# Kernel tuning notes

Measured on AMD Instinct MI355X. Metric: run time of the kernel, lower is better.

The kernel has to match this reference:

```python
import jax, jax.numpy as jnp
import numpy as np

H = 16        # num heads
DH = 128      # head dim
C = 64        # delta-rule chunk size
MAG = 0.5     # mag_weight
GATE_NORM = 16.0
EPS = 1e-6


def setup_inputs() -> dict:
    key = jax.random.key(0)
    ks = jax.random.split(key, 5)
    b, n, d = 2, 1024, H * DH
    s = d ** -0.5
    return {
        "x": jax.random.normal(ks[0], (b, n, d), jnp.float32),
        "Wq": jax.random.normal(ks[1], (d, d), jnp.float32) * s,
        "Wk": jax.random.normal(ks[2], (d, d), jnp.float32) * s,
        "Wv": jax.random.normal(ks[3], (d, d), jnp.float32) * s,
        "Wo": jax.random.normal(ks[4], (d, d), jnp.float32) * s,
    }


def _delta_rule_chunkwise(q, k, v, beta, chunk):
    # q,k,v: [b,h,l,d]; beta: [b,h,l,d] per-dim gate. Chunked DeltaNet parallel form.
    b, h, l, dk = q.shape
    dv = v.shape[-1]
    nc = l // chunk
    q = q * (dk ** -0.5)
    v = v * beta
    k_beta = k * beta
    qc, kc, vc, kbc = (a.reshape(b, h, nc, chunk, -1) for a in (q, k, v, k_beta))
    eye = jnp.eye(chunk, dtype=q.dtype)
    strict = jnp.tril(jnp.ones((chunk, chunk), bool), -1)
    # T = (I + strict_lower(k_beta k^T))^{-1} via triangular solve
    L = jnp.where(strict, kbc @ jnp.swapaxes(kc, -1, -2), 0.0)  # [b,h,nc,C,C]
    T = jax.scipy.linalg.solve_triangular(eye + L, jnp.broadcast_to(eye, L.shape), lower=True)
    u = T @ vc    # [b,h,nc,C,dv]
    w = T @ kbc   # [b,h,nc,C,dk]
    incl = jnp.tril(jnp.ones((chunk, chunk), bool))

    def step(S, inp):
        q_i, k_i, u_i, w_i = inp  # [b,h,C,d]
        u_i = u_i - w_i @ S
        attn = jnp.where(incl, q_i @ jnp.swapaxes(k_i, -1, -2), 0.0)
        o_i = q_i @ S + attn @ u_i
        S = S + jnp.swapaxes(k_i, -1, -2) @ u_i
        return S, o_i

    xs = tuple(jnp.moveaxis(a, 2, 0) for a in (qc, kc, u, w))
    S0 = jnp.zeros((b, h, dk, dv), q.dtype)
    S, o = jax.lax.scan(step, S0, xs)
    o = jnp.moveaxis(o, 0, 2).reshape(b, h, l, dv)
    return o, S


def _heads(t, b, n):
    return t.reshape(b, n, H, DH).transpose(0, 2, 1, 3)


def _base_attn(x, Wq, Wk, Wv, Wo):
    # vanilla causal softmax attention using the shared projections
    b, n, d = x.shape
    q, k, v = _heads(x @ Wq, b, n), _heads(x @ Wk, b, n), _heads(x @ Wv, b, n)
    scores = jnp.einsum('bhqd,bhkd->bhqk', q, k) / np.sqrt(DH).astype(np.float32)
    causal = jnp.tril(jnp.ones((n, n), bool))
    a = jax.nn.softmax(jnp.where(causal, scores, -jnp.inf), axis=-1)
    o = jnp.einsum('bhqk,bhkd->bhqd', a, v)
    return o.transpose(0, 2, 1, 3).reshape(b, n, d) @ Wo


def reference(x, Wq, Wk, Wv, Wo):
    b, n, d = x.shape
    k_raw = x @ Wk
    q = _heads(x @ Wq, b, n)
    k = _heads(k_raw, b, n)
    v = _heads(x @ Wv, b, n)
    g = _heads(k_raw, b, n)  # pool_g is identity: output_size == head_dim*num_kv_heads
    q = jnp.clip(jax.nn.softmax(q, axis=-1), EPS, 1.0 - EPS)
    k = jnp.clip(jax.nn.softmax(k, axis=-1), EPS, 1.0 - EPS)
    g = jnp.clip(jax.nn.log_sigmoid(g) / GATE_NORM, -GATE_NORM, GATE_NORM)
    o_lin, _ = _delta_rule_chunkwise(q.astype(jnp.float32), k.astype(jnp.float32),
                                     v.astype(jnp.float32), g.astype(jnp.float32), C)
    o_lin = o_lin.transpose(0, 2, 1, 3).reshape(b, n, d) @ Wo
    o_base = _base_attn(x, Wq, Wk, Wv, Wo)
    return MAG * o_lin + (1.0 - MAG) * o_base
```

## Files before the change

### kernel.cpp

```cpp
#include <hip/hip_runtime.h>
#include <hip/hip_bf16.h>
#include <math.h>

#define D 2048
#define NROWS 2048
#define NQKV 6144
#define H 16
#define DH 128
#define CHK 64
#define NC 16
#define EPSC 1e-6f
#define RSQDH 0.08838834764831845f

typedef unsigned short ushort_t;
typedef __attribute__((ext_vector_type(4))) float f4_t;
typedef __attribute__((ext_vector_type(8))) short s8_t;
typedef __attribute__((ext_vector_type(8))) _Float16 h8_t;
typedef __attribute__((ext_vector_type(4))) _Float16 h4_t;
typedef __attribute__((ext_vector_type(2))) _Float16 h2_t;
typedef __attribute__((ext_vector_type(4))) unsigned short us4_t;
typedef __attribute__((ext_vector_type(2))) unsigned short us2_t;

#define MFMA16(a, b, c) __builtin_amdgcn_mfma_f32_16x16x32_bf16((a), (b), (c), 0, 0, 0)
#define MFMAH(a, b, c)  __builtin_amdgcn_mfma_f32_16x16x32_f16((a), (b), (c), 0, 0, 0)
#define GLOAD16(g, l) __builtin_amdgcn_global_load_lds((const __attribute__((address_space(1))) unsigned int*)(g), (__attribute__((address_space(3))) unsigned int*)(l), 16, 0, 0)

__device__ __forceinline__ ushort_t f2bf(float f) {
  union { float f; unsigned u; } v; v.f = f;
  unsigned r = (v.u + 0x7fffu + ((v.u >> 16) & 1u)) >> 16;
  return (ushort_t)r;
}
__device__ __forceinline__ float bf2f(ushort_t h) {
  union { unsigned u; float f; } v; v.u = ((unsigned)h) << 16;
  return v.f;
}

__global__ __launch_bounds__(256) void split_h(const float* __restrict__ in,
                                               _Float16* __restrict__ hi) {
  int i = (blockIdx.x * 256 + threadIdx.x) * 4;
  float4 v = *(const float4*)(in + i);
  float vv[4] = {v.x, v.y, v.z, v.w};
  h4_t h;
#pragma unroll
  for (int j = 0; j < 4; j++) h[j] = (_Float16)vv[j];
  *(h4_t*)(hi + i) = h;
}

__global__ __launch_bounds__(256) void wsplit4(const float* __restrict__ Wq,
                                               const float* __restrict__ Wk,
                                               const float* __restrict__ Wv,
                                               const float* __restrict__ Wo,
                                               _Float16* __restrict__ Tqkv,
                                               _Float16* __restrict__ To) {
  __shared__ float t[32][33];
  const int tid = threadIdx.x;
  const int k0 = blockIdx.y * 32, n0 = blockIdx.x * 32;
  const int z = blockIdx.z;
  const float* W = (z == 0) ? Wq : (z == 1) ? Wk : (z == 2) ? Wv : Wo;
  _Float16* T = (z < 3) ? (Tqkv + (size_t)z * D * D) : To;
  const int c = tid & 31, rr = tid >> 5;
#pragma unroll
  for (int p = 0; p < 4; p++) {
    int r = p * 8 + rr;
    t[r][c] = W[(size_t)(k0 + r) * D + n0 + c];
  }
  __syncthreads();
#pragma unroll
  for (int p = 0; p < 4; p++) {
    int r = p * 8 + rr;
    T[(size_t)(n0 + r) * D + k0 + c] = (_Float16)t[c][r];
  }
}

__global__ __launch_bounds__(256) void gemm1(const _Float16* __restrict__ Ah,
                                             const _Float16* __restrict__ Bt,
                                             float* __restrict__ C,
                                             int M, int N, int K) {
  __shared__ __align__(16) ushort_t A_s[2][4096];
  __shared__ __align__(16) ushort_t B_s[2][4096];
  const int tid = threadIdx.x, lane = tid & 63, wid = tid >> 6;
  const int nwg = gridDim.x;
  int bid = blockIdx.x;
  int swz = (bid & 7) * (nwg >> 3) + (bid >> 3);
  const int nbn = N >> 7;
  const int bm = swz / nbn, bn = swz % nbn;
  const int row0 = bm << 7, col0 = bn << 7;
  const int lm = lane & 15, lg = lane >> 4;
  const int wrow = (wid >> 1) * 64, wcol = (wid & 1) * 64;
  const int NT = K >> 5;

  f4_t acc[4][4];
#pragma unroll
  for (int m = 0; m < 4; m++)
#pragma unroll
    for (int n = 0; n < 4; n++) acc[m][n] = (f4_t){0.f, 0.f, 0.f, 0.f};

  auto stage = [&](int buf, int ks) {
    int k0 = ks << 5;
#pragma unroll
    for (int p = 0; p < 2; p++) {
      int c = p * 256 + wid * 64 + lane;
      int r = c >> 2, q = (c & 3) * 8;
      char* la = (char*)&A_s[buf][0] + p * 4096 + wid * 1024;
      GLOAD16(Ah + (size_t)(row0 + r) * K + k0 + q, la);
      char* lb = (char*)&B_s[buf][0] + p * 4096 + wid * 1024;
      GLOAD16(Bt + (size_t)(col0 + r) * K + k0 + q, lb);
    }
  };

  stage(0, 0);
  __syncthreads();
  for (int t = 0; t < NT; t++) {
    int cur = t & 1;
    if (t + 1 < NT) stage(cur ^ 1, t + 1);
    h8_t af[4], bfr[4];
#pragma unroll
    for (int m = 0; m < 4; m++)
      af[m] = *(const h8_t*)&A_s[cur][(wrow + m * 16 + lm) * 32 + lg * 8];
#pragma unroll
    for (int n = 0; n < 4; n++)
      bfr[n] = *(const h8_t*)&B_s[cur][(wcol + n * 16 + lm) * 32 + lg * 8];
#pragma unroll
    for (int m = 0; m < 4; m++)
#pragma unroll
      for (int n = 0; n < 4; n++)
        acc[m][n] = MFMAH(af[m], bfr[n], acc[m][n]);
    __syncthreads();
  }
#pragma unroll
  for (int m = 0; m < 4; m++)
#pragma unroll
    for (int n = 0; n < 4; n++)
#pragma unroll
      for (int r = 0; r < 4; r++)
        C[(size_t)(row0 + wrow + m * 16 + lg * 4 + r) * N + col0 + wcol + n * 16 + lm] = acc[m][n][r];
}

__global__ __launch_bounds__(256) void gemm1h(const _Float16* __restrict__ Ah,
                                              const _Float16* __restrict__ Bt,
                                              _Float16* __restrict__ C,
                                              int M, int N, int K) {
  __shared__ __align__(16) ushort_t A_s[2][4096];
  __shared__ __align__(16) ushort_t B_s[2][4096];
  const int tid = threadIdx.x, lane = tid & 63, wid = tid >> 6;
  const int nwg = gridDim.x;
  int bid = blockIdx.x;
  int swz = (bid & 7) * (nwg >> 3) + (bid >> 3);
  const int nbn = N >> 7;
  const int bm = swz / nbn, bn = swz % nbn;
  const int lm = lane & 15, lg = lane >> 4;
  const int row0 = bm << 7, col0 = bn << 7;
  const int wrow = (wid >> 1) * 64, wcol = (wid & 1) * 64;
  const int NT = K >> 5;

  f4_t acc[4][4];
#pragma unroll
  for (int m = 0; m < 4; m++)
#pragma unroll
    for (int n = 0; n < 4; n++) acc[m][n] = (f4_t){0.f, 0.f, 0.f, 0.f};

  auto stage = [&](int buf, int ks) {
    int k0 = ks << 5;
#pragma unroll
    for (int p = 0; p < 2; p++) {
      int c = p * 256 + wid * 64 + lane;
      int r = c >> 2, q = (c & 3) * 8;
      char* la = (char*)&A_s[buf][0] + p * 4096 + wid * 1024;
      GLOAD16(Ah + (size_t)(row0 + r) * K + k0 + q, la);
      char* lb = (char*)&B_s[buf][0] + p * 4096 + wid * 1024;
      GLOAD16(Bt + (size_t)(col0 + r) * K + k0 + q, lb);
    }
  };

  stage(0, 0);
  __syncthreads();
  for (int t = 0; t < NT; t++) {
    int cur = t & 1;
    if (t + 1 < NT) stage(cur ^ 1, t + 1);
    h8_t af[4], bfr[4];
#pragma unroll
    for (int m = 0; m < 4; m++)
      af[m] = *(const h8_t*)&A_s[cur][(wrow + m * 16 + lm) * 32 + lg * 8];
#pragma unroll
    for (int n = 0; n < 4; n++)
      bfr[n] = *(const h8_t*)&B_s[cur][(wcol + n * 16 + lm) * 32 + lg * 8];
#pragma unroll
    for (int m = 0; m < 4; m++)
#pragma unroll
      for (int n = 0; n < 4; n++)
        acc[m][n] = MFMAH(af[m], bfr[n], acc[m][n]);
    __syncthreads();
  }
#pragma unroll
  for (int m = 0; m < 4; m++)
#pragma unroll
    for (int n = 0; n < 4; n++)
#pragma unroll
      for (int r = 0; r < 4; r++)
        C[(size_t)(row0 + wrow + m * 16 + lg * 4 + r) * N + col0 + wcol + n * 16 + lm] = (_Float16)acc[m][n][r];
}

__device__ __forceinline__ float gate_fn(float z) {
  float t = -z;
  float sp = (t > 20.f) ? t : log1pf(expf(t));
  float g = -sp * (1.f / 16.f);
  return fminf(fmaxf(g, -16.f), 16.f);
}

__global__ __launch_bounds__(256) void act_kernel(const _Float16* __restrict__ qkv,
                                                  ushort_t* __restrict__ qs_h,
                                                  ushort_t* __restrict__ qs_l,
                                                  float* __restrict__ ksm,
                                                  float* __restrict__ kb,
                                                  float* __restrict__ vb,
                                                  ushort_t* __restrict__ qb16,
                                                  ushort_t* __restrict__ kb16) {
  int wave = blockIdx.x * 4 + (threadIdx.x >> 6);
  int lane = threadIdx.x & 63;
  int row = wave >> 4, h = wave & 15;
  size_t inb = (size_t)row * NQKV + h * 128;
  size_t base = (size_t)wave * 128;
  const int e0 = 2 * lane;

  h2_t qv = *(const h2_t*)(qkv + inb + e0);
  h2_t kv = *(const h2_t*)(qkv + inb + 2048 + e0);
  h2_t vv = *(const h2_t*)(qkv + inb + 4096 + e0);
  float q0 = (float)qv[0], q1 = (float)qv[1];
  float k0 = (float)kv[0], k1 = (float)kv[1];
  float v0 = (float)vv[0], v1 = (float)vv[1];

  us2_t qo = {f2bf(q0 * RSQDH), f2bf(q1 * RSQDH)};
  us2_t ko = {f2bf(k0), f2bf(k1)};
  *(us2_t*)(qb16 + base + e0) = qo;
  *(us2_t*)(kb16 + base + e0) = ko;

  float m = fmaxf(q0, q1);
  for (int o = 1; o < 64; o <<= 1) m = fmaxf(m, __shfl_xor(m, o));
  float e0f = expf(q0 - m), e1f = expf(q1 - m);
  float s = e0f + e1f;
  for (int o = 1; o < 64; o <<= 1) s += __shfl_xor(s, o);
  float inv = 1.f / s;
  float qs0 = fminf(fmaxf(e0f * inv, EPSC), 1.f - EPSC) * RSQDH;
  float qs1 = fminf(fmaxf(e1f * inv, EPSC), 1.f - EPSC) * RSQDH;

  float mk = fmaxf(k0, k1);
  for (int o = 1; o < 64; o <<= 1) mk = fmaxf(mk, __shfl_xor(mk, o));
  float f0 = expf(k0 - mk), f1 = expf(k1 - mk);
  float sk = f0 + f1;
  for (int o = 1; o < 64; o <<= 1) sk += __shfl_xor(sk, o);
  float invk = 1.f / sk;
  float ks0 = fminf(fmaxf(f0 * invk, EPSC), 1.f - EPSC);
  float ks1 = fminf(fmaxf(f1 * invk, EPSC), 1.f - EPSC);

  float g0 = gate_fn(k0), g1 = gate_fn(k1);

  ushort_t qh0 = f2bf(qs0), qh1 = f2bf(qs1);
  us2_t qhv = {qh0, qh1};
  us2_t qlv = {f2bf(qs0 - bf2f(qh0)), f2bf(qs1 - bf2f(qh1))};
  *(us2_t*)(qs_h + base + e0) = qhv;
  *(us2_t*)(qs_l + base + e0) = qlv;

  *(float2*)(ksm + base + e0) = make_float2(ks0, ks1);
  *(float2*)(kb + base + e0) = make_float2(ks0 * g0, ks1 * g1);
  *(float2*)(vb + base + e0) = make_float2(v0 * g0, v1 * g1);
}

__global__ __launch_bounds__(256) void chunk_uw_kernel(const ushort_t* __restrict__ qs_h,
                                                       const ushort_t* __restrict__ qs_l,
                                                       const float* __restrict__ ksm,
                                                       const float* __restrict__ kb,
                                                       const float* __restrict__ vb,
                                                       float* __restrict__ u,
                                                       ushort_t* __restrict__ w_h,
                                                       ushort_t* __restrict__ w_l,
                                                       ushort_t* __restrict__ attn_h,
                                                       ushort_t* __restrict__ attn_l,
                                                       ushort_t* __restrict__ kTh_g,
                                                       ushort_t* __restrict__ kTl_g) {
  __shared__ __align__(16) ushort_t kh_s[8192];
  __shared__ __align__(16) ushort_t kl_s[8192];
  __shared__ __align__(16) ushort_t xh_s[8192];
  __shared__ __align__(16) ushort_t xl_s[8192];
  __shared__ float L_s[4096];
  const int tid = threadIdx.x, lane = tid & 63, wid = tid >> 6;
  const int lm = lane & 15, lg = lane >> 4;
  const int bh = blockIdx.x >> 4, ci = blockIdx.x & 15;
  const int rowbase = (bh >> 4) * 1024 + ci * 64;
  const int colbase = (bh & 15) * 128;
  const size_t gbase = (size_t)rowbase * D + colbase;
  const int wr = (wid >> 1) * 32, wc = (wid & 1) * 32;

  auto stageM = [&](const float* __restrict__ src, ushort_t* dh, ushort_t* dl) {
#pragma unroll
    for (int it = 0; it < 4; it++) {
      int idx = tid + it * 256;
      int r = idx >> 4, c8 = idx & 15;
      const float* g = src + gbase + (size_t)r * D + c8 * 8;
      float4 v0 = *(const float4*)g;
      float4 v1 = *(const float4*)(g + 4);
      float vv[8] = {v0.x, v0.y, v0.z, v0.w, v1.x, v1.y, v1.z, v1.w};
      s8_t hv, lv;
#pragma unroll
      for (int j = 0; j < 8; j++) {
        ushort_t hb = f2bf(vv[j]);
        hv[j] = (short)hb;
        lv[j] = (short)f2bf(vv[j] - bf2f(hb));
      }
      int byo = r * 256 + ((c8 * 16) ^ ((r & 7) << 4));
      *(s8_t*)((char*)dh + byo) = hv;
      *(s8_t*)((char*)dl + byo) = lv;
    }
  };

  auto stageHL = [&](const ushort_t* __restrict__ srcH,
                     const ushort_t* __restrict__ srcL,
                     ushort_t* dh, ushort_t* dl) {
#pragma unroll
    for (int it = 0; it < 4; it++) {
      int idx = tid + it * 256;
      int r = idx >> 4, c8 = idx & 15;
      size_t g = gbase + (size_t)r * D + c8 * 8;
      s8_t hv = *(const s8_t*)(srcH + g);
      s8_t lv = *(const s8_t*)(srcL + g);
      int byo = r * 256 + ((c8 * 16) ^ ((r & 7) << 4));
      *(s8_t*)((char*)dh + byo) = hv;
      *(s8_t*)((char*)dl + byo) = lv;
    }
  };

  auto mm3 = [&](const ushort_t* Ah, const ushort_t* Al,
                 const ushort_t* Bh, const ushort_t* Bl, f4_t acc[2][2]) {
#pragma unroll
    for (int m = 0; m < 2; m++)
#pragma unroll
      for (int n = 0; n < 2; n++) acc[m][n] = (f4_t){0.f, 0.f, 0.f, 0.f};
#pragma unroll
    for (int term = 0; term < 3; term++) {
      const ushort_t* A = (term == 2) ? Al : Ah;
      const ushort_t* Bsrc = (term == 1) ? Bl : Bh;
#pragma unroll
      for (int ks = 0; ks < 4; ks++) {
        s8_t af[2], bf_[2];
#pragma unroll
        for (int m = 0; m < 2; m++) {
          int row = wr + m * 16 + lm;
          int byo = row * 256 + ((ks * 64 + lg * 16) ^ ((row & 7) << 4));
          af[m] = *(const s8_t*)((const char*)A + byo);
        }
#pragma unroll
        for (int n = 0; n < 2; n++) {
          int row = wc + n * 16 + lm;
          int byo = row * 256 + ((ks * 64 + lg * 16) ^ ((row & 7) << 4));
          bf_[n] = *(const s8_t*)((const char*)Bsrc + byo);
        }
#pragma unroll
        for (int m = 0; m < 2; m++)
#pragma unroll
          for (int n = 0; n < 2; n++)
            acc[m][n] = MFMA16(af[m], bf_[n], acc[m][n]);
      }
    }
  };

  stageM(ksm, kh_s, kl_s);
  stageM(kb, xh_s, xl_s);
  __syncthreads();

  f4_t accL[2][2];
  mm3(xh_s, xl_s, kh_s, kl_s, accL);

  {
    const int dw = wid * 32;
    const int r = lane;
#pragma unroll
    for (int i = 0; i < 32; i++) {
      int d = dw + i;
      int byo = r * 256 + ((((d >> 3) ^ (r & 7)) << 4)) + (d & 7) * 2;
      ushort_t hv = *(const ushort_t*)((const char*)kh_s + byo);
      ushort_t lv = *(const ushort_t*)((const char*)kl_s + byo);
      size_t go = (size_t)(bh * 128 + d) * 1024 + ci * 64 + r;
      kTh_g[go] = hv;
      kTl_g[go] = lv;
    }
  }

#pragma unroll
  for (int m = 0; m < 2; m++)
#pragma unroll
    for (int n = 0; n < 2; n++)
#pragma unroll
      for (int r = 0; r < 4; r++) {
        int i = wr + m * 16 + lg * 4 + r;
        int j = wc + n * 16 + lm;
        L_s[i * 64 + j] = (j < i) ? accL[m][n][r] : 0.f;
      }
  __syncthreads();

  stageHL(qs_h, qs_l, xh_s, xl_s);
  __syncthreads();

  f4_t accA[2][2];
  mm3(xh_s, xl_s, kh_s, kl_s, accA);
  ushort_t* abh = attn_h + (size_t)blockIdx.x * 4096;
  ushort_t* abl = attn_l + (size_t)blockIdx.x * 4096;
#pragma unroll
  for (int m = 0; m < 2; m++)
#pragma unroll
    for (int n = 0; n < 2; n++)
#pragma unroll
      for (int r = 0; r < 4; r++) {
        int i = wr + m * 16 + lg * 4 + r;
        int j = wc + n * 16 + lm;
        float val = (j <= i) ? accA[m][n][r] : 0.f;
        ushort_t hb = f2bf(val);
        abh[i * 64 + j] = hb;
        abl[i * 64 + j] = f2bf(val - bf2f(hb));
      }

  float x[64];
  const int c = tid & 127;
  const float* rhs = (tid < 128) ? (vb + gbase + c) : (kb + gbase + c);
#pragma unroll
  for (int j = 0; j < 64; j++) x[j] = rhs[(size_t)j * D];
#pragma unroll
  for (int i = 0; i < 64; i++) {
    float xi = x[i];
#pragma unroll
    for (int r2 = i + 1; r2 < 64; r2++) x[r2] -= L_s[r2 * 64 + i] * xi;
  }
  if (tid < 128) {
#pragma unroll
    for (int j = 0; j < 64; j++) u[gbase + (size_t)j * D + c] = x[j];
  } else {
#pragma unroll
    for (int j = 0; j < 64; j++) {
      ushort_t hb = f2bf(x[j]);
      w_h[gbase + (size_t)j * D + c] = hb;
      w_l[gbase + (size_t)j * D + c] = f2bf(x[j] - bf2f(hb));
    }
  }
}

__global__ __launch_bounds__(512, 2) void scan_kernel(const ushort_t* __restrict__ qs_h,
                                                      const ushort_t* __restrict__ qs_l,
                                                      const float* __restrict__ u,
                                                      const ushort_t* __restrict__ w_h,
                                                      const ushort_t* __restrict__ w_l,
                                                      const ushort_t* __restrict__ kTh_g,
                                                      const ushort_t* __restrict__ kTl_g,
                                                      const ushort_t* __restrict__ ath_g,
                                                      const ushort_t* __restrict__ atl_g,
                                                      float* __restrict__ o_lin) {
  __shared__ __align__(16) ushort_t kT_h[2][8192];
  __shared__ __align__(16) ushort_t kT_l[2][8192];
  __shared__ __align__(16) ushort_t at_h[2][4096];
  __shared__ __align__(16) ushort_t at_l[2][4096];
  __shared__ __align__(16) ushort_t Sh_s[16 * 128];
  __shared__ __align__(16) ushort_t Sl_s[16 * 128];
  __shared__ __align__(16) ushort_t uh_s[16 * 80];
  __shared__ __align__(16) ushort_t ul_s[16 * 80];
  __shared__ __align__(16) float oT[16 * 68];
  const int tid = threadIdx.x;
  const int bh = blockIdx.x;
  const int b = bh >> 4, h = bh & 15;
  const int g = blockIdx.y;
  const int colbase = h * 128;
  const int vcol = h * 128 + g * 16;
  const int lane = tid & 63, wid = tid >> 6;
  const int lm = lane & 15, lg = lane >> 4;
  const int dsub = lane >> 3;
  const int i8x = (lane & 7) ^ dsub;

  for (int i = tid; i < 16 * 128; i += 512) { Sh_s[i] = 0; Sl_s[i] = 0; }

  f4_t acc3[2];
  acc3[0] = (f4_t){0.f, 0.f, 0.f, 0.f};
  acc3[1] = (f4_t){0.f, 0.f, 0.f, 0.f};

  const ushort_t* kThb = kTh_g + (size_t)bh * 128 * 1024;
  const ushort_t* kTlb = kTl_g + (size_t)bh * 128 * 1024;

  auto issue_stage = [&](int buf, int chunk) {
#pragma unroll
    for (int it = 0; it < 2; it++) {
      int seg = it * 8 + wid;
      int d = seg * 8 + dsub;
      size_t goff = (size_t)d * 1024 + chunk * 64 + i8x * 8;
      GLOAD16(kThb + goff, (char*)&kT_h[buf][0] + seg * 1024);
      GLOAD16(kTlb + goff, (char*)&kT_l[buf][0] + seg * 1024);
    }
    {
      int i = wid * 8 + dsub;
      size_t asrc = (size_t)(bh * 16 + chunk) * 4096 + i * 64 + i8x * 8;
      GLOAD16(ath_g + asrc, (char*)&at_h[buf][0] + wid * 1024);
      GLOAD16(atl_g + asrc, (char*)&at_l[buf][0] + wid * 1024);
    }
  };

  const bool isU = (wid < 4);
  const int m0 = (isU ? wid : (wid - 4)) * 16;
  const ushort_t* AsrcH = isU ? w_h : qs_h;
  const ushort_t* AsrcL = isU ? w_l : qs_l;

  s8_t pAh[4], pAl[4];
  float pu[4];
  auto prefetchA = [&](int chunk) {
    const size_t gb = (size_t)(b * 1024 + chunk * 64) * D;
#pragma unroll
    for (int ks = 0; ks < 4; ks++) {
      size_t off = gb + (size_t)(m0 + lm) * D + colbase + ks * 32 + lg * 8;
      pAh[ks] = *(const s8_t*)(AsrcH + off);
      pAl[ks] = *(const s8_t*)(AsrcL + off);
    }
    if (isU) {
#pragma unroll
      for (int r = 0; r < 4; r++)
        pu[r] = u[gb + (size_t)(m0 + lg * 4 + r) * D + vcol + lm];
    }
  };

  issue_stage(0, 0);
  prefetchA(0);
  __syncthreads();

  for (int chunk = 0; chunk < 16; chunk++) {
    const int cur = chunk & 1;
    const size_t gbase = (size_t)(b * 1024 + chunk * 64) * D;
    if (chunk + 1 < 16) issue_stage(cur ^ 1, chunk + 1);
    {
      f4_t acc = (f4_t){0.f, 0.f, 0.f, 0.f};
#pragma unroll
      for (int ks = 0; ks < 4; ks++) {
        int byo = (lm * 256 + ks * 64 + lg * 16) ^ ((lm & 7) << 4);
        s8_t sh = *(const s8_t*)((const char*)Sh_s + byo);
        s8_t sl = *(const s8_t*)((const char*)Sl_s + byo);
        acc = MFMA16(pAh[ks], sh, acc);
        acc = MFMA16(pAh[ks], sl, acc);
        acc = MFMA16(pAl[ks], sh, acc);
      }
      if (isU) {
        float res[4];
#pragma unroll
        for (int r = 0; r < 4; r++) res[r] = pu[r] - acc[r];
        us4_t rh, rl;
#pragma unroll
        for (int r = 0; r < 4; r++) {
          ushort_t hb = f2bf(res[r]);
          rh[r] = hb;
          rl[r] = f2bf(res[r] - bf2f(hb));
        }
        *(us4_t*)&uh_s[lm * 80 + m0 + lg * 4] = rh;
        *(us4_t*)&ul_s[lm * 80 + m0 + lg * 4] = rl;
      } else {
        float4 res = {acc[0], acc[1], acc[2], acc[3]};
        *(float4*)&oT[lm * 68 + m0 + lg * 4] = res;
      }
    }
    __syncthreads();
    if (chunk + 1 < 16) prefetchA(chunk + 1);
    if (isU) {
      float4 o0 = *(const float4*)&oT[lm * 68 + m0 + lg * 4];
      f4_t acc2 = (f4_t){o0.x, o0.y, o0.z, o0.w};
#pragma unroll
      for (int ks = 0; ks < 2; ks++) {
        int arow = m0 + lm;
        int abyo = arow * 128 + ((ks * 64 + lg * 16) ^ ((arow & 7) << 4));
        s8_t afh = *(const s8_t*)((const char*)&at_h[cur][0] + abyo);
        s8_t afl = *(const s8_t*)((const char*)&at_l[cur][0] + abyo);
        s8_t ufh = *(const s8_t*)&uh_s[lm * 80 + ks * 32 + lg * 8];
        s8_t ufl = *(const s8_t*)&ul_s[lm * 80 + ks * 32 + lg * 8];
        acc2 = MFMA16(afh, ufh, acc2);
        acc2 = MFMA16(afh, ufl, acc2);
        acc2 = MFMA16(afl, ufh, acc2);
      }
#pragma unroll
      for (int r = 0; r < 4; r++)
        o_lin[gbase + (size_t)(m0 + lg * 4 + r) * D + vcol + lm] = acc2[r];
    } else {
      const int w3 = wid - 4;
      s8_t ufh0 = *(const s8_t*)&uh_s[lm * 80 + 0 * 32 + lg * 8];
      s8_t ufl0 = *(const s8_t*)&ul_s[lm * 80 + 0 * 32 + lg * 8];
      s8_t ufh1 = *(const s8_t*)&uh_s[lm * 80 + 1 * 32 + lg * 8];
      s8_t ufl1 = *(const s8_t*)&ul_s[lm * 80 + 1 * 32 + lg * 8];
#pragma unroll
      for (int t = 0; t < 2; t++) {
        const int krow = (w3 * 2 + t) * 16 + lm;
        int b0 = krow * 128 + ((0 * 64 + lg * 16) ^ ((krow & 7) << 4));
        int b1 = krow * 128 + ((1 * 64 + lg * 16) ^ ((krow & 7) << 4));
        s8_t kh0 = *(const s8_t*)((const char*)&kT_h[cur][0] + b0);
        s8_t kl0 = *(const s8_t*)((const char*)&kT_l[cur][0] + b0);
        s8_t kh1 = *(const s8_t*)((const char*)&kT_h[cur][0] + b1);
        s8_t kl1 = *(const s8_t*)((const char*)&kT_l[cur][0] + b1);
        acc3[t] = MFMA16(ufh0, kh0, acc3[t]);
        acc3[t] = MFMA16(ufh0, kl0, acc3[t]);
        acc3[t] = MFMA16(ufl0, kh0, acc3[t]);
        acc3[t] = MFMA16(ufh1, kh1, acc3[t]);
        acc3[t] = MFMA16(ufh1, kl1, acc3[t]);
        acc3[t] = MFMA16(ufl1, kh1, acc3[t]);
      }
#pragma unroll
      for (int t = 0; t < 2; t++)
#pragma unroll
        for (int r = 0; r < 4; r++) {
          int c = lg * 4 + r;
          int k = (w3 * 2 + t) * 16 + lm;
          float sval = acc3[t][r];
          ushort_t hb = f2bf(sval);
          int sbyo = (c * 256 + k * 2) ^ ((c & 7) << 4);
          *(ushort_t*)((char*)Sh_s + sbyo) = hb;
          *(ushort_t*)((char*)Sl_s + sbyo) = f2bf(sval - bf2f(hb));
        }
    }
    __syncthreads();
  }
}

__global__ __launch_bounds__(256) void v_transpose(const _Float16* __restrict__ qkv,
                                                   ushort_t* __restrict__ vt) {
  __shared__ float t[32][33];
  const int tid = threadIdx.x;
  const int n0 = blockIdx.x * 32;
  const int d0 = blockIdx.y * 32;
  const int bh = blockIdx.z;
  const int b = bh >> 4, h = bh & 15;
  const int c = tid & 31, rr = tid >> 5;
#pragma unroll
  for (int p = 0; p < 4; p++) {
    int r = p * 8 + rr;
    t[r][c] = (float)qkv[(size_t)(b * 1024 + n0 + r) * NQKV + 4096 + h * 128 + d0 + c];
  }
  __syncthreads();
#pragma unroll
  for (int p = 0; p < 4; p++) {
    int r = p * 8 + rr;
    vt[(size_t)(bh * 128 + d0 + r) * 1024 + n0 + c] = f2bf(t[c][r]);
  }
}

__global__ __launch_bounds__(256) void attn_mfma(const ushort_t* __restrict__ qb,
                                                 const ushort_t* __restrict__ kb,
                                                 const ushort_t* __restrict__ vt,
                                                 const float* __restrict__ o_lin,
                                                 _Float16* __restrict__ mixh) {
  __shared__ __align__(16) ushort_t K_s[8192];
  __shared__ __align__(16) ushort_t V_s[8192];
  __shared__ __align__(16) ushort_t P_s[4][1152];
  const int tid = threadIdx.x;
  const int lane = tid & 63, wid = tid >> 6;
  const int bh = blockIdx.x;
  const int b = bh >> 4, h = bh & 15;
  const int qt = (int)(gridDim.y - 1) - (int)blockIdx.y;
  const int lm = lane & 15, lg = lane >> 4;

  s8_t qf[4];
  const size_t qrowG = (size_t)(b * 1024 + qt * 64 + wid * 16 + lm);
#pragma unroll
  for (int kb4 = 0; kb4 < 4; kb4++)
    qf[kb4] = *(const s8_t*)(qb + qrowG * D + h * 128 + kb4 * 32 + lg * 8);

  f4_t o[8];
#pragma unroll
  for (int n = 0; n < 8; n++) o[n] = (f4_t){0.f, 0.f, 0.f, 0.f};
  float mrow[4] = {-INFINITY, -INFINITY, -INFINITY, -INFINITY};
  float lrow[4] = {0.f, 0.f, 0.f, 0.f};
  const int myq = qt * 64 + wid * 16 + lg * 4;

  for (int kt = 0; kt <= qt; kt++) {
    __syncthreads();
#pragma unroll
    for (int p = 0; p < 4; p++) {
      int c = tid + p * 256;
      int key = c >> 4, dc = c & 15;
      s8_t v = *(const s8_t*)(kb + (size_t)(b * 1024 + kt * 64 + key) * D + h * 128 + dc * 8);
      int byo = key * 256 + ((dc * 16) ^ ((key & 7) << 4));
      *(s8_t*)((char*)K_s + byo) = v;
    }
#pragma unroll
    for (int p = 0; p < 4; p++) {
      int c = tid + p * 256;
      int d = c >> 3, nc = c & 7;
      s8_t v = *(const s8_t*)(vt + (size_t)(bh * 128 + d) * 1024 + kt * 64 + nc * 8);
      int byo = d * 128 + ((nc * 16) ^ ((d & 7) << 4));
      *(s8_t*)((char*)V_s + byo) = v;
    }
    __syncthreads();

    f4_t s[4];
#pragma unroll
    for (int ks = 0; ks < 4; ks++) {
      f4_t a = (f4_t){0.f, 0.f, 0.f, 0.f};
      int key = ks * 16 + lm;
#pragma unroll
      for (int kb4 = 0; kb4 < 4; kb4++) {
        int byo = key * 256 + ((kb4 * 64 + lg * 16) ^ ((key & 7) << 4));
        s8_t kf = *(const s8_t*)((char*)K_s + byo);
        a = MFMA16(qf[kb4], kf, a);
      }
      s[ks] = a;
    }
    if (kt == qt) {
#pragma unroll
      for (int ks = 0; ks < 4; ks++) {
        int key = kt * 64 + ks * 16 + lm;
#pragma unroll
        for (int r = 0; r < 4; r++)
          if (key > myq + r) s[ks][r] = -INFINITY;
      }
    }
    float mloc[4];
#pragma unroll
    for (int r = 0; r < 4; r++) {
      mloc[r] = fmaxf(fmaxf(s[0][r], s[1][r]), fmaxf(s[2][r], s[3][r]));
      mloc[r] = fmaxf(mloc[r], __shfl_xor(mloc[r], 1));
      mloc[r] = fmaxf(mloc[r], __shfl_xor(mloc[r], 2));
      mloc[r] = fmaxf(mloc[r], __shfl_xor(mloc[r], 4));
      mloc[r] = fmaxf(mloc[r], __shfl_xor(mloc[r], 8));
    }
    float scale[4];
#pragma unroll
    for (int r = 0; r < 4; r++) {
      float mn = fmaxf(mrow[r], mloc[r]);
      scale[r] = __expf(mrow[r] - mn);
      mrow[r] = mn;
    }
    float lad[4] = {0.f, 0.f, 0.f, 0.f};
#pragma unroll
    for (int ks = 0; ks < 4; ks++)
#pragma unroll
      for (int r = 0; r < 4; r++) {
        float p = __expf(s[ks][r] - mrow[r]);
        lad[r] += p;
        P_s[wid][(lg * 4 + r) * 72 + ks * 16 + lm] = f2bf(p);
      }
#pragma unroll
    for (int r = 0; r < 4; r++) {
      lad[r] += __shfl_xor(lad[r], 1);
      lad[r] += __shfl_xor(lad[r], 2);
      lad[r] += __shfl_xor(lad[r], 4);
      lad[r] += __shfl_xor(lad[r], 8);
      lrow[r] = lrow[r] * scale[r] + lad[r];
    }
#pragma unroll
    for (int n = 0; n < 8; n++)
#pragma unroll
      for (int r = 0; r < 4; r++) o[n][r] *= scale[r];

    s8_t pf[2];
#pragma unroll
    for (int ksl = 0; ksl < 2; ksl++)
      pf[ksl] = *(const s8_t*)&P_s[wid][lm * 72 + ksl * 32 + lg * 8];
#pragma unroll
    for (int n = 0; n < 8; n++) {
      int d = n * 16 + lm;
#pragma unroll
      for (int ksl = 0; ksl < 2; ksl++) {
        int byo = d * 128 + ((ksl * 64 + lg * 16) ^ ((d & 7) << 4));
        s8_t vf = *(const s8_t*)((char*)V_s + byo);
        o[n] = MFMA16(pf[ksl], vf, o[n]);
      }
    }
  }

  float invl[4];
#pragma unroll
  for (int r = 0; r < 4; r++) invl[r] = 1.f / lrow[r];
#pragma unroll
  for (int n = 0; n < 8; n++)
#pragma unroll
    for (int r = 0; r < 4; r++) {
      size_t G = (size_t)(b * 1024 + qt * 64 + wid * 16 + lg * 4 + r);
      int dcol = h * 128 + n * 16 + lm;
      float mix = 0.5f * (o[n][r] * invl[r]) + 0.5f * o_lin[G * D + dcol];
      mixh[G * D + dcol] = (_Float16)mix;
    }
}

extern "C" void kernel_launch(void* const* d_in, const int* in_sizes, int n_in,
                              void* d_out, int out_size, void* d_ws, size_t ws_size,
                              hipStream_t stream) {
  const float* x  = (const float*)d_in[0];
  const float* Wq = (const float*)d_in[1];
  const float* Wk = (const float*)d_in[2];
  const float* Wv = (const float*)d_in[3];
  const float* Wo = (const float*)d_in[4];
  float* out = (float*)d_out;
  float* ws = (float*)d_ws;

  const size_t B = (size_t)NROWS * D;
  _Float16* qkv = (_Float16*)(ws + 0 * B);
  float* q_s  = ws + 3 * B;
  float* k_sm = ws + 4 * B;
  float* kbuf = ws + 5 * B;
  float* vbuf = ws + 6 * B;
  float* u    = ws + 7 * B;
  float* w    = ws + 8 * B;
  float* o_lin = kbuf;

  _Float16* x_hi = (_Float16*)u;
  _Float16* Wt   = (_Float16*)(ws + 9 * B);
  ushort_t* attn_h = (ushort_t*)(ws + 9 * B);
  ushort_t* attn_l = attn_h + (size_t)2097152;
  ushort_t* kTh_g  = (ushort_t*)(ws + 9 * B + 2097152);
  ushort_t* kTl_g  = (ushort_t*)(ws + 10 * B);
  _Float16* Wo_t   = (_Float16*)(ws + 10 * B + 2097152);
  ushort_t* qs_h = (ushort_t*)q_s;
  ushort_t* qs_l = qs_h + B;
  ushort_t* w_h  = (ushort_t*)w;
  ushort_t* w_l  = w_h + B;
  ushort_t* qb16 = (ushort_t*)(ws + 2 * B);
  ushort_t* kb16 = qb16 + B;
  ushort_t* vt16 = (ushort_t*)vbuf;
  _Float16* mixh = (_Float16*)qkv;

  split_h<<<4096, 256, 0, stream>>>(x, x_hi);
  wsplit4<<<dim3(64, 64, 4), 256, 0, stream>>>(Wq, Wk, Wv, Wo, Wt, Wo_t);
  gemm1h<<<16 * 48, 256, 0, stream>>>(x_hi, Wt, qkv, NROWS, NQKV, D);

  act_kernel<<<8192, 256, 0, stream>>>(qkv, qs_h, qs_l, k_sm, kbuf, vbuf, qb16, kb16);
  chunk_uw_kernel<<<512, 256, 0, stream>>>(qs_h, qs_l, k_sm, kbuf, vbuf, u, w_h, w_l,
                                           attn_h, attn_l, kTh_g, kTl_g);
  scan_kernel<<<dim3(32, 8), 512, 0, stream>>>(qs_h, qs_l, u, w_h, w_l, kTh_g, kTl_g, attn_h, attn_l, o_lin);

  v_transpose<<<dim3(32, 4, 32), 256, 0, stream>>>(qkv, vt16);
  attn_mfma<<<dim3(32, 16), 256, 0, stream>>>(qb16, kb16, vt16, o_lin, mixh);

  gemm1<<<16 * 16, 256, 0, stream>>>(mixh, Wo_t, out, NROWS, D, D);
}
```

Measured before the change: 277.7 us.

## Prefetch next K/V tile into registers and skip rescale with lazy max

The causal attention loop now loads the next key/value tile from global memory into registers while the current tile is being computed, then writes it to shared memory at the top of the next iteration. This hides global load latency behind the QK and PV MFMAs, at the cost of extra registers. The softmax online rescaling is also made lazy: the running max and the rescale of o and l only update when some row's new max exceeds the stored one by more than 8, skipping the exp and multiplies most iterations. The threshold lets probabilities grow up to e^8 before rescaling, which could affect bf16 precision of P.

```diff
diff --git a/kernel.cpp b/kernel.cpp
--- a/kernel.cpp
+++ b/kernel.cpp
@@ -665,25 +665,43 @@
   float lrow[4] = {0.f, 0.f, 0.f, 0.f};
   const int myq = qt * 64 + wid * 16 + lg * 4;
 
-  for (int kt = 0; kt <= qt; kt++) {
-    __syncthreads();
+  s8_t sK[4], sV[4];
+  auto loadK = [&](int kt) {
 #pragma unroll
     for (int p = 0; p < 4; p++) {
       int c = tid + p * 256;
       int key = c >> 4, dc = c & 15;
-      s8_t v = *(const s8_t*)(kb + (size_t)(b * 1024 + kt * 64 + key) * D + h * 128 + dc * 8);
-      int byo = key * 256 + ((dc * 16) ^ ((key & 7) << 4));
-      *(s8_t*)((char*)K_s + byo) = v;
-    }
+      sK[p] = *(const s8_t*)(kb + (size_t)(b * 1024 + kt * 64 + key) * D + h * 128 + dc * 8);
+    }
+  };
+  auto loadV = [&](int kt) {
 #pragma unroll
     for (int p = 0; p < 4; p++) {
       int c = tid + p * 256;
       int d = c >> 3, nc = c & 7;
-      s8_t v = *(const s8_t*)(vt + (size_t)(bh * 128 + d) * 1024 + kt * 64 + nc * 8);
-      int byo = d * 128 + ((nc * 16) ^ ((d & 7) << 4));
-      *(s8_t*)((char*)V_s + byo) = v;
-    }
+      sV[p] = *(const s8_t*)(vt + (size_t)(bh * 128 + d) * 1024 + kt * 64 + nc * 8);
+    }
+  };
+  auto writeKV = [&]() {
+#pragma unroll
+    for (int p = 0; p < 4; p++) {
+      int c = tid + p * 256;
+      int key = c >> 4, dc = c & 15;
+      int byo = key * 256 + ((dc * 16) ^ ((key & 7) << 4));
+      *(s8_t*)((char*)K_s + byo) = sK[p];
+      int d = c >> 3, nc = c & 7;
+      int byo2 = d * 128 + ((nc * 16) ^ ((d & 7) << 4));
+      *(s8_t*)((char*)V_s + byo2) = sV[p];
+    }
+  };
+
+  loadK(0);
+  loadV(0);
+
+  for (int kt = 0; kt <= qt; kt++) {
+    writeKV();
     __syncthreads();
+    if (kt < qt) { loadK(kt + 1); loadV(kt + 1); }
 
     f4_t s[4];
 #pragma unroll
@@ -716,12 +734,23 @@
       mloc[r] = fmaxf(mloc[r], __shfl_xor(mloc[r], 4));
       mloc[r] = fmaxf(mloc[r], __shfl_xor(mloc[r], 8));
     }
-    float scale[4];
-#pragma unroll
-    for (int r = 0; r < 4; r++) {
-      float mn = fmaxf(mrow[r], mloc[r]);
-      scale[r] = __expf(mrow[r] - mn);
-      mrow[r] = mn;
+    int grow = 0;
+#pragma unroll
+    for (int r = 0; r < 4; r++)
+      grow |= (mloc[r] > mrow[r] + 8.f) ? 1 : 0;
+    if (__any(grow)) {
+      float scale[4];
+#pragma unroll
+      for (int r = 0; r < 4; r++) {
+        float mn = fmaxf(mrow[r], mloc[r]);
+        scale[r] = __expf(mrow[r] - mn);
+        mrow[r] = mn;
+        lrow[r] *= scale[r];
+      }
+#pragma unroll
+      for (int n = 0; n < 8; n++)
+#pragma unroll
+        for (int r = 0; r < 4; r++) o[n][r] *= scale[r];
     }
     float lad[4] = {0.f, 0.f, 0.f, 0.f};
 #pragma unroll
@@ -738,12 +767,8 @@
       lad[r] += __shfl_xor(lad[r], 2);
       lad[r] += __shfl_xor(lad[r], 4);
       lad[r] += __shfl_xor(lad[r], 8);
-      lrow[r] = lrow[r] * scale[r] + lad[r];
-    }
-#pragma unroll
-    for (int n = 0; n < 8; n++)
-#pragma unroll
-      for (int r = 0; r < 4; r++) o[n][r] *= scale[r];
+      lrow[r] += lad[r];
+    }
 
     s8_t pf[2];
 #pragma unroll
@@ -759,6 +784,7 @@
         o[n] = MFMA16(pf[ksl], vf, o[n]);
       }
     }
+    __syncthreads();
   }
 
   float invl[4];
```

Result: no change. 275.7 us (-0.7%).
